# Kernel tuning notes

Hardware: AMD Instinct MI355X
Metric: run time of the kernel (lower is better)

The kernel has to match this reference:

```python
import math
import jax, jax.numpy as jnp
import numpy as np

DIM = 2048
N_HEADS = 16
HEAD_DIM = DIM // N_HEADS  # 128
BSZ = 2
SEQLEN = 2048
ROPE_THETA = 500000.0


def _make_freqs(seqlen, head_dim, theta):
    inv = 1.0 / (theta ** (np.arange(0, head_dim, 2, dtype=np.float32) / head_dim))
    t = np.arange(seqlen, dtype=np.float32)
    f = np.outer(t, inv)  # [S, hd//2]
    return jnp.asarray(np.cos(f)), jnp.asarray(np.sin(f))


def setup_inputs() -> dict:
    key = jax.random.key(0)
    kx, kq, kk, kv, ko = jax.random.split(key, 5)
    scale = 0.02
    x = jax.random.normal(kx, (BSZ, SEQLEN, DIM), dtype=jnp.float32)
    wq = jax.random.normal(kq, (DIM, DIM), dtype=jnp.float32) * scale
    wk = jax.random.normal(kk, (DIM, DIM), dtype=jnp.float32) * scale
    wv = jax.random.normal(kv, (DIM, DIM), dtype=jnp.float32) * scale
    wo = jax.random.normal(ko, (DIM, DIM), dtype=jnp.float32) * scale
    freqs_cos, freqs_sin = _make_freqs(SEQLEN, HEAD_DIM, ROPE_THETA)
    # causal additive mask: 0 on/below diag, -inf above
    mask = jnp.triu(jnp.full((SEQLEN, SEQLEN), float('-inf'), dtype=jnp.float32), k=1)
    return {"x": x, "start_pos": 0, "freqs_cos": freqs_cos, "freqs_sin": freqs_sin,
            "mask": mask, "wq": wq, "wk": wk, "wv": wv, "wo": wo}


def _apply_rope(t, cos, sin):
    # t: [B, S, H, hd]; cos/sin: [S, hd//2]
    b, s, h, hd = t.shape
    tr = t.reshape(b, s, h, hd // 2, 2)
    a, bb = tr[..., 0], tr[..., 1]
    c = cos[None, :, None, :]
    sn = sin[None, :, None, :]
    out_r = a * c - bb * sn
    out_i = a * sn + bb * c
    return jnp.stack([out_r, out_i], axis=-1).reshape(b, s, h, hd)


def reference(x, start_pos, freqs_cos, freqs_sin, mask, wq, wk, wv, wo):
    b, s, _ = x.shape
    xq = (x @ wq.T).reshape(b, s, N_HEADS, HEAD_DIM)
    xk = (x @ wk.T).reshape(b, s, N_HEADS, HEAD_DIM)
    xv = (x @ wv.T).reshape(b, s, N_HEADS, HEAD_DIM)
    xq = _apply_rope(xq, freqs_cos, freqs_sin)
    xk = _apply_rope(xk, freqs_cos, freqs_sin)
    # [B, H, S, hd]
    xq = xq.transpose(0, 2, 1, 3)
    xk = xk.transpose(0, 2, 1, 3)
    xv = xv.transpose(0, 2, 1, 3)
    scores = jnp.einsum('bhqd,bhkd->bhqk', xq, xk) / math.sqrt(HEAD_DIM)
    scores = scores + mask[None, None, :, :]
    probs = jax.nn.softmax(scores.astype(jnp.float32), axis=-1).astype(xq.dtype)
    out = jnp.einsum('bhqk,bhkd->bhqd', probs, xv)
    out = out.transpose(0, 2, 1, 3).reshape(b, s, -1)
    return out @ wo.T
```

## Files before the change

kernel.cpp:

```cpp
#include <hip/hip_runtime.h>
#include <stdint.h>

#define DIM 2048
#define SEQ 2048
#define NHEADS 16
#define HDIM 128
#define BSZ 2
#define ROWS (BSZ*SEQ)

typedef uint16_t u16;
typedef __attribute__((ext_vector_type(8))) short bf16x8;
typedef __attribute__((ext_vector_type(4))) short bf16x4;
typedef __attribute__((ext_vector_type(4))) float fx4;
typedef __attribute__((ext_vector_type(4))) uint16_t u16x4;

typedef const __attribute__((address_space(1))) uint32_t* gp_t;
typedef __attribute__((address_space(3))) uint32_t* lp_t;
#define GLL16(g, l) __builtin_amdgcn_global_load_lds((gp_t)(g), (lp_t)(l), 16, 0, 0)

__device__ inline u16 f2bf(float f) {
  union { float f; uint32_t u; } v; v.f = f;
  uint32_t u = v.u;
  u += 0x7FFFu + ((u >> 16) & 1u);
  return (u16)(u >> 16);
}
__device__ inline float bf2f(u16 h) {
  union { uint32_t u; float f; } v; v.u = ((uint32_t)h) << 16;
  return v.f;
}

__global__ __launch_bounds__(256) void cvt5_kernel(const float* __restrict__ sx,
    const float* __restrict__ s1, const float* __restrict__ s2,
    const float* __restrict__ s3, const float* __restrict__ s4,
    u16* __restrict__ dst) {
  const int XC = (ROWS * DIM) / 4;
  const int WC = (DIM * DIM) / 4;
  int i = blockIdx.x * 256 + threadIdx.x;
  const float* src;
  int off;
  if (i < XC) { src = sx; off = i; }
  else {
    int t = i - XC;
    int w = t >> 20;
    off = t & (WC - 1);
    src = (w == 0) ? s1 : (w == 1) ? s2 : (w == 2) ? s3 : s4;
  }
  fx4 f = *(const fx4*)(src + (size_t)off * 4);
  u16x4 o;
  o[0] = f2bf(f[0]); o[1] = f2bf(f[1]); o[2] = f2bf(f[2]); o[3] = f2bf(f[3]);
  *(u16x4*)(dst + (size_t)i * 4) = o;
}

__device__ inline void gemm128_core(const u16* __restrict__ A, const u16* __restrict__ B,
                                    u16 (&As)[128][32], u16 (&Bs)[128][32],
                                    fx4 (&acc)[4][4], int M0, int N0) {
  const int tid  = threadIdx.x;
  const int lane = tid & 63;
  const int wave = tid >> 6;
  const int wm = (wave >> 1) * 64;
  const int wn = (wave & 1) * 64;
  const int l16 = lane & 15;
  const int q8  = (lane >> 4) * 8;
#pragma unroll
  for (int tm = 0; tm < 4; ++tm)
#pragma unroll
    for (int tn = 0; tn < 4; ++tn) acc[tm][tn] = fx4{0.f, 0.f, 0.f, 0.f};

  const int wrow = wave * 32;
  const size_t laneA = (size_t)(M0 + wrow + (lane >> 2)) * DIM + (lane & 3) * 8;
  const size_t laneB = (size_t)(N0 + wrow + (lane >> 2)) * DIM + (lane & 3) * 8;

  for (int k0 = 0; k0 < DIM; k0 += 32) {
    __syncthreads();
    GLL16(A + laneA + k0,            &As[wrow][0]);
    GLL16(A + laneA + 16 * DIM + k0, &As[wrow + 16][0]);
    GLL16(B + laneB + k0,            &Bs[wrow][0]);
    GLL16(B + laneB + 16 * DIM + k0, &Bs[wrow + 16][0]);
    __syncthreads();
    bf16x8 af[4], bfr[4];
#pragma unroll
    for (int t = 0; t < 4; ++t) {
      af[t]  = *(const bf16x8*)&As[wm + t * 16 + l16][q8];
      bfr[t] = *(const bf16x8*)&Bs[wn + t * 16 + l16][q8];
    }
#pragma unroll
    for (int tm = 0; tm < 4; ++tm)
#pragma unroll
      for (int tn = 0; tn < 4; ++tn)
        acc[tm][tn] = __builtin_amdgcn_mfma_f32_16x16x32_bf16(af[tm], bfr[tn], acc[tm][tn], 0, 0, 0);
  }
}

__global__ __launch_bounds__(256) void gemm_qkv(const u16* __restrict__ A,
    const u16* __restrict__ B0, const u16* __restrict__ B1, const u16* __restrict__ B2,
    u16* __restrict__ C0, u16* __restrict__ C1, u16* __restrict__ C2) {
  __shared__ __align__(16) u16 As[128][32];
  __shared__ __align__(16) u16 Bs[128][32];
  const u16* B = (blockIdx.z == 0) ? B0 : (blockIdx.z == 1) ? B1 : B2;
  u16* C       = (blockIdx.z == 0) ? C0 : (blockIdx.z == 1) ? C1 : C2;
  const int M0 = blockIdx.y * 128, N0 = blockIdx.x * 128;
  fx4 acc[4][4];
  gemm128_core(A, B, As, Bs, acc, M0, N0);
  const int lane = threadIdx.x & 63, wave = threadIdx.x >> 6;
  const int wm = (wave >> 1) * 64, wn = (wave & 1) * 64;
  const int l16 = lane & 15, quad = lane >> 4;
#pragma unroll
  for (int tm = 0; tm < 4; ++tm)
#pragma unroll
    for (int tn = 0; tn < 4; ++tn)
#pragma unroll
      for (int r = 0; r < 4; ++r) {
        size_t row = (size_t)(M0 + wm + tm * 16 + quad * 4 + r);
        size_t col = (size_t)(N0 + wn + tn * 16 + l16);
        C[row * DIM + col] = f2bf(acc[tm][tn][r]);
      }
}

__global__ __launch_bounds__(256) void gemm_out(const u16* __restrict__ A,
                                                const u16* __restrict__ B,
                                                float* __restrict__ C) {
  __shared__ __align__(16) u16 As[128][32];
  __shared__ __align__(16) u16 Bs[128][32];
  const int M0 = blockIdx.y * 128, N0 = blockIdx.x * 128;
  fx4 acc[4][4];
  gemm128_core(A, B, As, Bs, acc, M0, N0);
  const int lane = threadIdx.x & 63, wave = threadIdx.x >> 6;
  const int wm = (wave >> 1) * 64, wn = (wave & 1) * 64;
  const int l16 = lane & 15, quad = lane >> 4;
#pragma unroll
  for (int tm = 0; tm < 4; ++tm)
#pragma unroll
    for (int tn = 0; tn < 4; ++tn)
#pragma unroll
      for (int r = 0; r < 4; ++r) {
        size_t row = (size_t)(M0 + wm + tm * 16 + quad * 4 + r);
        size_t col = (size_t)(N0 + wn + tn * 16 + l16);
        C[row * DIM + col] = acc[tm][tn][r];
      }
}

__global__ __launch_bounds__(256) void rope_kernel(u16* __restrict__ q, u16* __restrict__ k,
                                                   const float* __restrict__ fcos,
                                                   const float* __restrict__ fsin) {
  int idx = blockIdx.x * 256 + threadIdx.x;
  int t = idx >> 22;
  int p_all = idx & ((1 << 22) - 1);
  u16* ptr = t ? k : q;
  int row = p_all >> 10;
  int r   = p_all & 1023;
  int h   = r >> 6;
  int p   = r & 63;
  int s   = row & (SEQ - 1);
  size_t base = (size_t)row * DIM + h * HDIM + 2 * p;
  float a = bf2f(ptr[base]), b = bf2f(ptr[base + 1]);
  float c = fcos[s * 64 + p], sn = fsin[s * 64 + p];
  ptr[base]     = f2bf(a * c - b * sn);
  ptr[base + 1] = f2bf(a * sn + b * c);
}

__global__ __launch_bounds__(256) void vtrans_kernel(const u16* __restrict__ v,
                                                     u16* __restrict__ vtg) {
  __shared__ __align__(16) u16 T[128][72];
  const int tid = threadIdx.x;
  const int s0 = blockIdx.x * 64;
  const int bh = blockIdx.y;
  const int b = bh >> 4, h = bh & 15;
  const size_t vb = ((size_t)b * SEQ + s0) * DIM + h * HDIM;
#pragma unroll
  for (int i = 0; i < 4; ++i) {
    int c = i * 256 + tid;
    int s = c >> 4;
    int d0 = (c & 15) * 8;
    bf16x8 x = *(const bf16x8*)(v + vb + (size_t)s * DIM + d0);
#pragma unroll
    for (int j = 0; j < 8; ++j) T[d0 + j][s] = (u16)x[j];
  }
  __syncthreads();
  const size_t ob = ((size_t)bh * HDIM) * SEQ + s0;
#pragma unroll
  for (int i = 0; i < 4; ++i) {
    int c = i * 256 + tid;
    int d = c >> 3;
    int s8 = (c & 7) * 8;
    *(bf16x8*)(vtg + ob + (size_t)d * SEQ + s8) = *(const bf16x8*)&T[d][s8];
  }
}

struct SMemS { u16 Ks[64][136]; u16 Vt[128][72]; };
union SMemU { SMemS s; u16 Ot[4][32][136]; };

__global__ __launch_bounds__(256, 2) void attn_kernel(const u16* __restrict__ qm,
                                                      const u16* __restrict__ km,
                                                      const u16* __restrict__ vtg,
                                                      u16* __restrict__ ao) {
  __shared__ __align__(16) SMemU sm;
  const int tid = threadIdx.x;
  const int lane = tid & 63, wave = tid >> 6;
  const int l16 = lane & 15, quad = lane >> 4;
  const int idx = blockIdx.x;
  const int bh = idx & 31;
  const int j = idx >> 5;
  const int qt = (j < 8) ? (15 - j) : (j - 8);
  const int b = bh >> 4, h = bh & 15;
  const int q0 = qt * 128;
  const size_t brow = (size_t)b * SEQ;
  const int hc = h * HDIM;
  const size_t vbase = (size_t)bh * HDIM * SEQ;
  const int nkt = 2 * qt + 2;

  bf16x8 aq[2][4];
#pragma unroll
  for (int nt = 0; nt < 2; ++nt) {
    size_t qbase = (brow + q0 + wave * 32 + nt * 16 + l16) * DIM + hc;
#pragma unroll
    for (int dc = 0; dc < 4; ++dc)
      aq[nt][dc] = *(const bf16x8*)(qm + qbase + dc * 32 + quad * 8);
  }
  fx4 o[2][8];
#pragma unroll
  for (int nt = 0; nt < 2; ++nt)
#pragma unroll
    for (int dt = 0; dt < 8; ++dt) o[nt][dt] = fx4{0.f, 0.f, 0.f, 0.f};
  float mr[2] = {-3e38f, -3e38f}, lr[2] = {0.f, 0.f};

  bf16x8 kreg[4], vreg[4];
#pragma unroll
  for (int i = 0; i < 4; ++i) {
    int c = i * 256 + tid;
    kreg[i] = *(const bf16x8*)(km + (brow + (c >> 4)) * DIM + hc + (c & 15) * 8);
    vreg[i] = *(const bf16x8*)(vtg + vbase + (size_t)(c >> 3) * SEQ + (c & 7) * 8);
  }

  for (int kt = 0; kt < nkt; ++kt) {
    __syncthreads();
#pragma unroll
    for (int i = 0; i < 4; ++i) {
      int c = i * 256 + tid;
      *(bf16x8*)&sm.s.Ks[c >> 4][(c & 15) * 8] = kreg[i];
      *(bf16x8*)&sm.s.Vt[c >> 3][(c & 7) * 8] = vreg[i];
    }
    __syncthreads();
    if (kt + 1 < nkt) {
      const int kv1 = (kt + 1) * 64;
#pragma unroll
      for (int i = 0; i < 4; ++i) {
        int c = i * 256 + tid;
        kreg[i] = *(const bf16x8*)(km + (brow + kv1 + (c >> 4)) * DIM + hc + (c & 15) * 8);
        vreg[i] = *(const bf16x8*)(vtg + vbase + (size_t)(c >> 3) * SEQ + kv1 + (c & 7) * 8);
      }
    }
    fx4 s[2][4];
#pragma unroll
    for (int tm = 0; tm < 4; ++tm) {
      fx4 a0 = fx4{0.f, 0.f, 0.f, 0.f}, a1 = fx4{0.f, 0.f, 0.f, 0.f};
#pragma unroll
      for (int dc = 0; dc < 4; ++dc) {
        bf16x8 kf = *(const bf16x8*)&sm.s.Ks[tm * 16 + l16][dc * 32 + quad * 8];
        a0 = __builtin_amdgcn_mfma_f32_16x16x32_bf16(kf, aq[0][dc], a0, 0, 0, 0);
        a1 = __builtin_amdgcn_mfma_f32_16x16x32_bf16(kf, aq[1][dc], a1, 0, 0, 0);
      }
      s[0][tm] = a0 * 0.08838834764831845f;
      s[1][tm] = a1 * 0.08838834764831845f;
    }
    if (kt >= nkt - 2) {
      const int kv0 = kt * 64;
#pragma unroll
      for (int nt = 0; nt < 2; ++nt) {
        int qpos = q0 + wave * 32 + nt * 16 + l16;
#pragma unroll
        for (int tm = 0; tm < 4; ++tm)
#pragma unroll
          for (int r = 0; r < 4; ++r)
            if (kv0 + tm * 16 + quad * 4 + r > qpos) s[nt][tm][r] = -1e30f;
      }
    }
    float alpha[2];
    bf16x4 pf[2][4];
#pragma unroll
    for (int nt = 0; nt < 2; ++nt) {
      float t = -3e38f;
#pragma unroll
      for (int tm = 0; tm < 4; ++tm)
        t = fmaxf(t, fmaxf(fmaxf(s[nt][tm][0], s[nt][tm][1]),
                           fmaxf(s[nt][tm][2], s[nt][tm][3])));
      t = fmaxf(t, __shfl_xor(t, 16));
      t = fmaxf(t, __shfl_xor(t, 32));
      float mnew = fmaxf(mr[nt], t);
      alpha[nt] = __expf(mr[nt] - mnew);
      float sum = 0.f;
#pragma unroll
      for (int tm = 0; tm < 4; ++tm) {
        fx4 p;
#pragma unroll
        for (int r = 0; r < 4; ++r) {
          p[r] = __expf(s[nt][tm][r] - mnew);
          sum += p[r];
        }
        bf16x4 pb;
        pb[0] = (short)f2bf(p[0]); pb[1] = (short)f2bf(p[1]);
        pb[2] = (short)f2bf(p[2]); pb[3] = (short)f2bf(p[3]);
        pf[nt][tm] = pb;
      }
      sum += __shfl_xor(sum, 16);
      sum += __shfl_xor(sum, 32);
      lr[nt] = lr[nt] * alpha[nt] + sum;
      mr[nt] = mnew;
#pragma unroll
      for (int dt = 0; dt < 8; ++dt) o[nt][dt] *= alpha[nt];
    }
#pragma unroll
    for (int tm = 0; tm < 4; ++tm) {
#pragma unroll
      for (int dt = 0; dt < 8; ++dt) {
        bf16x4 vf = *(const bf16x4*)&sm.s.Vt[dt * 16 + l16][tm * 16 + quad * 4];
        o[0][dt] = __builtin_amdgcn_mfma_f32_16x16x16bf16_1k(vf, pf[0][tm], o[0][dt], 0, 0, 0);
        o[1][dt] = __builtin_amdgcn_mfma_f32_16x16x16bf16_1k(vf, pf[1][tm], o[1][dt], 0, 0, 0);
      }
    }
  }
  __syncthreads();
#pragma unroll
  for (int nt = 0; nt < 2; ++nt) {
    float inv = 1.f / lr[nt];
#pragma unroll
    for (int dt = 0; dt < 8; ++dt) {
      fx4 v = o[nt][dt];
      u16x4 p;
      p[0] = f2bf(v[0] * inv); p[1] = f2bf(v[1] * inv);
      p[2] = f2bf(v[2] * inv); p[3] = f2bf(v[3] * inv);
      *(u16x4*)&sm.Ot[wave][nt * 16 + l16][dt * 16 + quad * 4] = p;
    }
  }
#pragma unroll
  for (int i = 0; i < 8; ++i) {
    int c = i * 64 + lane;
    int row = c >> 4;
    int ch = c & 15;
    bf16x8 t = *(const bf16x8*)&sm.Ot[wave][row][ch * 8];
    *(bf16x8*)(ao + (brow + q0 + wave * 32 + row) * DIM + hc + ch * 8) = t;
  }
}

extern "C" void kernel_launch(void* const* d_in, const int* in_sizes, int n_in,
                              void* d_out, int out_size, void* d_ws, size_t ws_size,
                              hipStream_t stream) {
  const float* x    = (const float*)d_in[0];
  const float* fcos = (const float*)d_in[2];
  const float* fsin = (const float*)d_in[3];
  const float* wq   = (const float*)d_in[5];
  const float* wk   = (const float*)d_in[6];
  const float* wv   = (const float*)d_in[7];
  const float* wo   = (const float*)d_in[8];
  float* out = (float*)d_out;

  const size_t XN = (size_t)ROWS * DIM;
  const size_t WN = (size_t)DIM * DIM;
  u16* ws  = (u16*)d_ws;
  u16* xb  = ws;
  u16* wqb = xb + XN;
  u16* wkb = wqb + WN;
  u16* wvb = wkb + WN;
  u16* wob = wvb + WN;
  u16* q   = wob + WN;
  u16* k   = q + XN;
  u16* v   = k + XN;
  u16* ao  = v + XN;
  u16* vtg = xb;

  const int total_chunks = (int)((XN + 4 * WN) / 4);
  cvt5_kernel<<<total_chunks / 256, 256, 0, stream>>>(x, wq, wk, wv, wo, ws);

  gemm_qkv<<<dim3(DIM / 128, ROWS / 128, 3), 256, 0, stream>>>(xb, wqb, wkb, wvb, q, k, v);

  rope_kernel<<<2 * ROWS * 1024 / 256, 256, 0, stream>>>(q, k, fcos, fsin);
  vtrans_kernel<<<dim3(SEQ / 64, BSZ * NHEADS), 256, 0, stream>>>(v, vtg);

  attn_kernel<<<dim3(512), 256, 0, stream>>>(q, k, vtg, ao);

  gemm_out<<<dim3(DIM / 128, ROWS / 128), 256, 0, stream>>>(ao, wob, out);
}
```

Before: 427.2 us.

## Rewrite QKV GEMM with 256x256 tiles, double-buffered async LDS loads and swizzle

Replaces the 128x128 QKV projection GEMM with a 512-thread kernel that computes 256x256 output tiles with BK=64. Global-to-LDS loads are double-buffered and interleaved with four MFMA quadrant phases, and the LDS layout is XOR-swizzled to avoid bank conflicts. Blocks are remapped across XCDs and raised priority is set during MFMA bursts. The goal is better operand reuse and overlap of memory with compute. In exchange it uses a large register budget and many barriers, and relies on delicate manual waitcnt ordering.

```diff
diff --git a/kernel.cpp b/kernel.cpp
--- a/kernel.cpp
+++ b/kernel.cpp
@@ -91,29 +91,157 @@
   }
 }
 
-__global__ __launch_bounds__(256) void gemm_qkv(const u16* __restrict__ A,
+#define BM 256
+#define BN 256
+#define BK 64
+#define NT (DIM / BK)
+
+__global__ __launch_bounds__(512, 2) void gemm_qkv8(const u16* __restrict__ A,
     const u16* __restrict__ B0, const u16* __restrict__ B1, const u16* __restrict__ B2,
     u16* __restrict__ C0, u16* __restrict__ C1, u16* __restrict__ C2) {
-  __shared__ __align__(16) u16 As[128][32];
-  __shared__ __align__(16) u16 Bs[128][32];
-  const u16* B = (blockIdx.z == 0) ? B0 : (blockIdx.z == 1) ? B1 : B2;
-  u16* C       = (blockIdx.z == 0) ? C0 : (blockIdx.z == 1) ? C1 : C2;
-  const int M0 = blockIdx.y * 128, N0 = blockIdx.x * 128;
-  fx4 acc[4][4];
-  gemm128_core(A, B, As, Bs, acc, M0, N0);
-  const int lane = threadIdx.x & 63, wave = threadIdx.x >> 6;
-  const int wm = (wave >> 1) * 64, wn = (wave & 1) * 64;
-  const int l16 = lane & 15, quad = lane >> 4;
-#pragma unroll
-  for (int tm = 0; tm < 4; ++tm)
-#pragma unroll
-    for (int tn = 0; tn < 4; ++tn)
-#pragma unroll
-      for (int r = 0; r < 4; ++r) {
-        size_t row = (size_t)(M0 + wm + tm * 16 + quad * 4 + r);
-        size_t col = (size_t)(N0 + wn + tn * 16 + l16);
-        C[row * DIM + col] = f2bf(acc[tm][tn][r]);
-      }
+  __shared__ __align__(16) u16 sm[2 * 2 * BM * BK];
+
+  const int tid  = threadIdx.x;
+  const int lane = tid & 63, wave = tid >> 6;
+  const int l16  = lane & 15, quad = lane >> 4;
+  const int wm   = wave >> 2;
+  const int wn   = wave & 3;
+
+  int t = (blockIdx.x & 7) * 48 + (blockIdx.x >> 3);
+  const int z   = t >> 7;
+  const int rem = t & 127;
+  const int M0  = (rem >> 3) * BM;
+  const int N0  = (rem & 7) * BN;
+  const u16* B = (z == 0) ? B0 : (z == 1) ? B1 : B2;
+  u16* C       = (z == 0) ? C0 : (z == 1) ? C1 : C2;
+
+  const int u0 = tid, u1 = 512 + tid;
+  const int rl0 = u0 >> 3, ch0 = (u0 & 7) ^ (rl0 & 7);
+  const int rl1 = u1 >> 3, ch1 = (u1 & 7) ^ (rl1 & 7);
+
+  const int sw  = l16 & 7;
+  const int ka0 = (quad ^ sw) * 8;
+  const int ka1 = ((4 + quad) ^ sw) * 8;
+  const int rowA = (wm * 128 + l16) * BK;
+  const int rowB = (wn * 64  + l16) * BK;
+
+#define STG(gb, R0, o, h, kt2) do { if ((kt2) < NT) {                                    \
+    const u16* _g = (gb) + (size_t)((R0) + (h) * 128) * DIM + (kt2) * BK;                \
+    u16* _l = sm + (((kt2) & 1) * 2 + (o)) * (BM * BK) + (h) * (128 * BK) + wave * 512;  \
+    GLL16(_g + (size_t)rl0 * DIM + ch0 * 8, _l);                                         \
+    GLL16(_g + (size_t)rl1 * DIM + ch1 * 8, _l + 4096); } } while (0)
+
+  STG(B, N0, 1, 0, 0); STG(A, M0, 0, 0, 0);
+  STG(B, N0, 1, 1, 0); STG(A, M0, 0, 1, 0);
+  STG(B, N0, 1, 0, 1); STG(A, M0, 0, 0, 1);
+  asm volatile("s_waitcnt vmcnt(4)" ::: "memory");
+  __builtin_amdgcn_s_barrier();
+
+  fx4 acc[8][4];
+#pragma unroll
+  for (int m = 0; m < 8; ++m)
+#pragma unroll
+    for (int n = 0; n < 4; ++n) acc[m][n] = fx4{0.f, 0.f, 0.f, 0.f};
+
+  bf16x8 af[4][2], bl[2][2], bh[2][2];
+
+  for (int kt = 0; kt < NT; ++kt) {
+    const u16* Ab = sm + ((kt & 1) * 2 + 0) * (BM * BK);
+    const u16* Bb = sm + ((kt & 1) * 2 + 1) * (BM * BK);
+
+#pragma unroll
+    for (int m = 0; m < 4; ++m) {
+      af[m][0] = *(const bf16x8*)(Ab + rowA + m * (16 * BK) + ka0);
+      af[m][1] = *(const bf16x8*)(Ab + rowA + m * (16 * BK) + ka1);
+    }
+#pragma unroll
+    for (int n = 0; n < 2; ++n) {
+      bl[n][0] = *(const bf16x8*)(Bb + rowB + n * (16 * BK) + ka0);
+      bl[n][1] = *(const bf16x8*)(Bb + rowB + n * (16 * BK) + ka1);
+    }
+    STG(B, N0, 1, 1, kt + 1);
+    asm volatile("s_waitcnt lgkmcnt(8)" ::: "memory");
+    __builtin_amdgcn_sched_barrier(0);
+    __builtin_amdgcn_s_barrier();
+    asm volatile("s_waitcnt lgkmcnt(0)" ::: "memory");
+    __builtin_amdgcn_sched_barrier(0);
+    __builtin_amdgcn_s_setprio(1);
+#pragma unroll
+    for (int m = 0; m < 4; ++m)
+#pragma unroll
+      for (int n = 0; n < 2; ++n) {
+        acc[m][n] = __builtin_amdgcn_mfma_f32_16x16x32_bf16(af[m][0], bl[n][0], acc[m][n], 0, 0, 0);
+        acc[m][n] = __builtin_amdgcn_mfma_f32_16x16x32_bf16(af[m][1], bl[n][1], acc[m][n], 0, 0, 0);
+      }
+    __builtin_amdgcn_s_setprio(0);
+    __builtin_amdgcn_s_barrier();
+
+#pragma unroll
+    for (int n = 0; n < 2; ++n) {
+      bh[n][0] = *(const bf16x8*)(Bb + rowB + (n + 2) * (16 * BK) + ka0);
+      bh[n][1] = *(const bf16x8*)(Bb + rowB + (n + 2) * (16 * BK) + ka1);
+    }
+    STG(A, M0, 0, 1, kt + 1);
+    __builtin_amdgcn_s_barrier();
+    asm volatile("s_waitcnt lgkmcnt(0)" ::: "memory");
+    __builtin_amdgcn_sched_barrier(0);
+    __builtin_amdgcn_s_setprio(1);
+#pragma unroll
+    for (int m = 0; m < 4; ++m)
+#pragma unroll
+      for (int n = 0; n < 2; ++n) {
+        acc[m][n + 2] = __builtin_amdgcn_mfma_f32_16x16x32_bf16(af[m][0], bh[n][0], acc[m][n + 2], 0, 0, 0);
+        acc[m][n + 2] = __builtin_amdgcn_mfma_f32_16x16x32_bf16(af[m][1], bh[n][1], acc[m][n + 2], 0, 0, 0);
+      }
+    __builtin_amdgcn_s_setprio(0);
+    __builtin_amdgcn_s_barrier();
+
+#pragma unroll
+    for (int m = 0; m < 4; ++m) {
+      af[m][0] = *(const bf16x8*)(Ab + rowA + (m + 4) * (16 * BK) + ka0);
+      af[m][1] = *(const bf16x8*)(Ab + rowA + (m + 4) * (16 * BK) + ka1);
+    }
+    STG(B, N0, 1, 0, kt + 2);
+    __builtin_amdgcn_s_barrier();
+    asm volatile("s_waitcnt lgkmcnt(0)" ::: "memory");
+    __builtin_amdgcn_sched_barrier(0);
+    __builtin_amdgcn_s_setprio(1);
+#pragma unroll
+    for (int m = 0; m < 4; ++m)
+#pragma unroll
+      for (int n = 0; n < 2; ++n) {
+        acc[m + 4][n + 2] = __builtin_amdgcn_mfma_f32_16x16x32_bf16(af[m][0], bh[n][0], acc[m + 4][n + 2], 0, 0, 0);
+        acc[m + 4][n + 2] = __builtin_amdgcn_mfma_f32_16x16x32_bf16(af[m][1], bh[n][1], acc[m + 4][n + 2], 0, 0, 0);
+      }
+    __builtin_amdgcn_s_setprio(0);
+    __builtin_amdgcn_s_barrier();
+
+    STG(A, M0, 0, 0, kt + 2);
+    __builtin_amdgcn_s_barrier();
+    __builtin_amdgcn_s_setprio(1);
+#pragma unroll
+    for (int m = 0; m < 4; ++m)
+#pragma unroll
+      for (int n = 0; n < 2; ++n) {
+        acc[m + 4][n] = __builtin_amdgcn_mfma_f32_16x16x32_bf16(af[m][0], bl[n][0], acc[m + 4][n], 0, 0, 0);
+        acc[m + 4][n] = __builtin_amdgcn_mfma_f32_16x16x32_bf16(af[m][1], bl[n][1], acc[m + 4][n], 0, 0, 0);
+      }
+    __builtin_amdgcn_s_setprio(0);
+    if (kt < NT - 2) asm volatile("s_waitcnt vmcnt(4)" ::: "memory");
+    else             asm volatile("s_waitcnt vmcnt(0)" ::: "memory");
+    __builtin_amdgcn_sched_barrier(0);
+    __builtin_amdgcn_s_barrier();
+  }
+#undef STG
+
+  u16* Cr = C + (size_t)(M0 + wm * 128 + quad * 4) * DIM + N0 + wn * 64 + l16;
+#pragma unroll
+  for (int mt = 0; mt < 8; ++mt)
+#pragma unroll
+    for (int nt = 0; nt < 4; ++nt)
+#pragma unroll
+      for (int r = 0; r < 4; ++r)
+        Cr[(size_t)(mt * 16 + r) * DIM + nt * 16] = f2bf(acc[mt][nt][r]);
 }
 
 __global__ __launch_bounds__(256) void gemm_out(const u16* __restrict__ A,
@@ -370,7 +498,7 @@
   const int total_chunks = (int)((XN + 4 * WN) / 4);
   cvt5_kernel<<<total_chunks / 256, 256, 0, stream>>>(x, wq, wk, wv, wo, ws);
 
-  gemm_qkv<<<dim3(DIM / 128, ROWS / 128, 3), 256, 0, stream>>>(xb, wqb, wkb, wvb, q, k, v);
+  gemm_qkv8<<<dim3(384), 512, 0, stream>>>(xb, wqb, wkb, wvb, q, k, v);
 
   rope_kernel<<<2 * ROWS * 1024 / 256, 256, 0, stream>>>(q, k, fcos, fsin);
   vtrans_kernel<<<dim3(SEQ / 64, BSZ * NHEADS), 256, 0, stream>>>(v, vtg);
```

After: 417.6 us. -2.3%, faster.
